# Kernel tuning notes

Hardware: AMD Instinct MI355X
Metric: run time of the kernel (lower is better)

Reference implementation:

```python
import jax, jax.numpy as jnp
import numpy as np

N_NODES = 50000
N_EDGES = 800000
IN_FEATS = 128
OUT_FEATS = 128


def setup_inputs() -> dict:
    key = jax.random.key(0)
    k1, k2, k3, k4 = jax.random.split(key, 4)
    feature = jax.random.normal(k1, (N_NODES, IN_FEATS), dtype=jnp.float32)
    src = jax.random.randint(k2, (N_EDGES,), 0, N_NODES, dtype=jnp.int64)
    dst = jax.random.randint(k3, (N_EDGES,), 0, N_NODES, dtype=jnp.int64)
    # nn.Linear(in_feats, out_feats): W is [out, in], b is [out]
    bound = 1.0 / np.sqrt(IN_FEATS)
    W = jax.random.uniform(k4, (OUT_FEATS, IN_FEATS), minval=-bound, maxval=bound, dtype=jnp.float32)
    b = jnp.zeros((OUT_FEATS,), dtype=jnp.float32)
    return {"feature": feature, "src": src, "dst": dst, "W": W, "b": b}


def reference(feature, src, dst, W, b):
    # DGL update_all(copy_src('h'), sum('m','h')): h'[v] = sum over edges u->v of h[u]
    n_nodes = feature.shape[0]
    msgs = feature[src]  # [E, in_feats] gather
    agg = jax.ops.segment_sum(msgs, dst, num_segments=n_nodes)  # [N, in_feats]
    # linear: agg @ W.T + b
    return jnp.einsum("ni,oi->no", agg, W) + b
```

## Files before the change

kernel.cpp:

```cpp
#include <hip/hip_runtime.h>
#include <hip/hip_bf16.h>

#define N_FEATS 128
#define SCAN_CHUNK 1024

typedef __attribute__((ext_vector_type(8))) short bf16x8;
typedef __attribute__((ext_vector_type(4))) float f32x4;

__device__ __forceinline__ unsigned short f32_to_bf16_rne(float f) {
    unsigned u = __float_as_uint(f);
    u = u + 0x7FFFu + ((u >> 16) & 1u);
    return (unsigned short)(u >> 16);
}

__global__ void gcn_init(const float* __restrict__ W, unsigned short* __restrict__ Wb,
                         int* __restrict__ deg, int n_nodes) {
    int t = blockIdx.x * blockDim.x + threadIdx.x;
    if (t < N_FEATS * N_FEATS / 8) {
        const float4* f4 = reinterpret_cast<const float4*>(W) + (size_t)t * 2;
        float4 x0 = f4[0];
        float4 x1 = f4[1];
        ushort4 o0, o1;
        o0.x = f32_to_bf16_rne(x0.x); o0.y = f32_to_bf16_rne(x0.y);
        o0.z = f32_to_bf16_rne(x0.z); o0.w = f32_to_bf16_rne(x0.w);
        o1.x = f32_to_bf16_rne(x1.x); o1.y = f32_to_bf16_rne(x1.y);
        o1.z = f32_to_bf16_rne(x1.z); o1.w = f32_to_bf16_rne(x1.w);
        reinterpret_cast<ushort4*>(Wb)[(size_t)t * 2 + 0] = o0;
        reinterpret_cast<ushort4*>(Wb)[(size_t)t * 2 + 1] = o1;
    }
    int u = t - N_FEATS * N_FEATS / 8;
    if (u >= 0 && u < n_nodes) deg[u] = 0;
}

__launch_bounds__(256)
__global__ void gcn_transform_mfma(const float* __restrict__ feat,
                                   const unsigned short* __restrict__ Wb,
                                   unsigned short* __restrict__ Y,
                                   int n_nodes) {
    const long long gtid = (long long)blockIdx.x * blockDim.x + threadIdx.x;
    const int wave = (int)(gtid >> 6);
    const int row0 = wave * 16;
    if (row0 >= n_nodes) return;
    const int l = (int)(threadIdx.x & 63);
    const int lr = l & 15;
    const int kb = l >> 4;

    bf16x8 afrag[4] = {};
    if (row0 + lr < n_nodes) {
        const float* aptr = feat + (size_t)(row0 + lr) * N_FEATS + kb * 8;
#pragma unroll
        for (int kk = 0; kk < 4; ++kk) {
            float4 x0 = *reinterpret_cast<const float4*>(aptr + kk * 32);
            float4 x1 = *reinterpret_cast<const float4*>(aptr + kk * 32 + 4);
            bf16x8 af;
            af[0] = (short)f32_to_bf16_rne(x0.x);
            af[1] = (short)f32_to_bf16_rne(x0.y);
            af[2] = (short)f32_to_bf16_rne(x0.z);
            af[3] = (short)f32_to_bf16_rne(x0.w);
            af[4] = (short)f32_to_bf16_rne(x1.x);
            af[5] = (short)f32_to_bf16_rne(x1.y);
            af[6] = (short)f32_to_bf16_rne(x1.z);
            af[7] = (short)f32_to_bf16_rne(x1.w);
            afrag[kk] = af;
        }
    }

    f32x4 acc[8];
#pragma unroll
    for (int nt = 0; nt < 8; ++nt) acc[nt] = (f32x4){0.f, 0.f, 0.f, 0.f};

#pragma unroll
    for (int nt = 0; nt < 8; ++nt) {
        const unsigned short* wp = Wb + (size_t)(nt * 16 + lr) * N_FEATS + kb * 8;
#pragma unroll
        for (int kk = 0; kk < 4; ++kk) {
            bf16x8 bfrag = *reinterpret_cast<const bf16x8*>(wp + kk * 32);
            acc[nt] = __builtin_amdgcn_mfma_f32_16x16x32_bf16(afrag[kk], bfrag, acc[nt], 0, 0, 0);
        }
    }

#pragma unroll
    for (int nt = 0; nt < 8; ++nt) {
        const int col = nt * 16 + lr;
#pragma unroll
        for (int j = 0; j < 4; ++j) {
            const int r = row0 + kb * 4 + j;
            if (r < n_nodes)
                Y[(size_t)r * N_FEATS + col] = f32_to_bf16_rne(acc[nt][j]);
        }
    }
}

__global__ void gcn_hist_pos(const int* __restrict__ src, const int* __restrict__ dst,
                             int* __restrict__ deg, int* __restrict__ pos,
                             int n_edges, int n_nodes) {
    int e = blockIdx.x * blockDim.x + threadIdx.x;
    if (e >= n_edges) return;
    int d = dst[e];
    int s = src[e];
    if ((unsigned)d < (unsigned)n_nodes && (unsigned)s < (unsigned)n_nodes)
        pos[e] = atomicAdd(&deg[d], 1);
}

__launch_bounds__(256)
__global__ void gcn_scan(const int* __restrict__ deg, int* __restrict__ row_start,
                         int n, int nchunks) {
    const int t = threadIdx.x;
    const int b = blockIdx.x;
    const int base = b * SCAN_CHUNK;

    int v = 0;
    for (int j = t; j < base; j += 256) v += deg[j];
    for (int d = 1; d < 64; d <<= 1) v += __shfl_xor(v, d, 64);
    __shared__ int owsum[4];
    __shared__ int s_off;
    if ((t & 63) == 0) owsum[t >> 6] = v;
    __syncthreads();
    if (t == 0) s_off = owsum[0] + owsum[1] + owsum[2] + owsum[3];
    __syncthreads();
    const int chunk_off = s_off;

    const int idx0 = base + t * 4;
    int x[4];
#pragma unroll
    for (int k = 0; k < 4; ++k) {
        int idx = idx0 + k;
        x[k] = (idx < n) ? deg[idx] : 0;
    }
    const int tsum = x[0] + x[1] + x[2] + x[3];

    const int lane = t & 63, w = t >> 6;
    int inc = tsum;
    for (int d = 1; d < 64; d <<= 1) {
        int sv = __shfl_up(inc, d, 64);
        if (lane >= d) inc += sv;
    }
    __shared__ int wsum[4];
    if (lane == 63) wsum[w] = inc;
    __syncthreads();
    int woff = 0;
    for (int i = 0; i < w; ++i) woff += wsum[i];

    int run = chunk_off + woff + inc - tsum;
#pragma unroll
    for (int k = 0; k < 4; ++k) {
        int idx = idx0 + k;
        if (idx < n) row_start[idx] = run;
        run += x[k];
    }

    if (t == 0 && b == nchunks - 1)
        row_start[n] = chunk_off + wsum[0] + wsum[1] + wsum[2] + wsum[3];
}

__global__ void gcn_build_csr_pos(const int* __restrict__ src, const int* __restrict__ dst,
                                  const int* __restrict__ row_start, const int* __restrict__ pos,
                                  int* __restrict__ csr_src, int n_edges, int n_nodes) {
    int e = blockIdx.x * blockDim.x + threadIdx.x;
    if (e >= n_edges) return;
    int d = dst[e];
    int s = src[e];
    if ((unsigned)d >= (unsigned)n_nodes || (unsigned)s >= (unsigned)n_nodes) return;
    csr_src[row_start[d] + pos[e]] = s;
}

#define BACC(acc, v)                                              \
    do {                                                          \
        unsigned uu;                                              \
        uu = (v).x;                                               \
        acc[0] += __uint_as_float(uu << 16);                      \
        acc[1] += __uint_as_float(uu & 0xFFFF0000u);              \
        uu = (v).y;                                               \
        acc[2] += __uint_as_float(uu << 16);                      \
        acc[3] += __uint_as_float(uu & 0xFFFF0000u);              \
        uu = (v).z;                                               \
        acc[4] += __uint_as_float(uu << 16);                      \
        acc[5] += __uint_as_float(uu & 0xFFFF0000u);              \
        uu = (v).w;                                               \
        acc[6] += __uint_as_float(uu << 16);                      \
        acc[7] += __uint_as_float(uu & 0xFFFF0000u);              \
    } while (0)

__launch_bounds__(256)
__global__ void gcn_aggregate_bf16(const uint4* __restrict__ Y,
                                   const int* __restrict__ row_start,
                                   const int* __restrict__ csr_src,
                                   const float* __restrict__ bias,
                                   float* __restrict__ out, int n_nodes) {
    int node = blockIdx.x * 4 + (threadIdx.x >> 6);
    if (node >= n_nodes) return;
    const int l = threadIdx.x & 63;
    const int qw = l >> 4;
    const int ql = l & 15;
    int beg = row_start[node];
    int end = row_start[node + 1];

    float a0[8] = {0,0,0,0,0,0,0,0};
    float a1[8] = {0,0,0,0,0,0,0,0};
    float a2[8] = {0,0,0,0,0,0,0,0};
    float a3[8] = {0,0,0,0,0,0,0,0};

    int i = beg;
    for (; i + 16 <= end; i += 16) {
        int s0 = csr_src[i + qw];
        int s1 = csr_src[i + 4 + qw];
        int s2 = csr_src[i + 8 + qw];
        int s3 = csr_src[i + 12 + qw];
        uint4 v0 = Y[(size_t)s0 * 16 + ql];
        uint4 v1 = Y[(size_t)s1 * 16 + ql];
        uint4 v2 = Y[(size_t)s2 * 16 + ql];
        uint4 v3 = Y[(size_t)s3 * 16 + ql];
        BACC(a0, v0);
        BACC(a1, v1);
        BACC(a2, v2);
        BACC(a3, v3);
    }
    for (; i + 4 <= end; i += 4) {
        int s = csr_src[i + qw];
        uint4 v = Y[(size_t)s * 16 + ql];
        BACC(a0, v);
    }
    int rem = end - i;
    if (qw < rem) {
        int s = csr_src[i + qw];
        uint4 v = Y[(size_t)s * 16 + ql];
        BACC(a0, v);
    }

    float r[8];
#pragma unroll
    for (int k = 0; k < 8; ++k) {
        r[k] = a0[k] + a1[k] + a2[k] + a3[k];
        r[k] += __shfl_xor(r[k], 16, 64);
        r[k] += __shfl_xor(r[k], 32, 64);
    }

    if (qw == 0) {
        const float4 b0 = *reinterpret_cast<const float4*>(bias + ql * 8);
        const float4 b1 = *reinterpret_cast<const float4*>(bias + ql * 8 + 4);
        float4* o4 = reinterpret_cast<float4*>(out + (size_t)node * N_FEATS + ql * 8);
        o4[0] = make_float4(r[0] + b0.x, r[1] + b0.y, r[2] + b0.z, r[3] + b0.w);
        o4[1] = make_float4(r[4] + b1.x, r[5] + b1.y, r[6] + b1.z, r[7] + b1.w);
    }
}

__global__ void gcn_init_c(const float* __restrict__ W, float* __restrict__ Wt) {
    int t = blockIdx.x * blockDim.x + threadIdx.x;
    if (t < N_FEATS * N_FEATS) {
        int o = t >> 7;
        int i = t & 127;
        Wt[i * N_FEATS + o] = W[o * N_FEATS + i];
    }
}

__global__ void gcn_scatter_add(const float* __restrict__ feat,
                                const int* __restrict__ src,
                                const int* __restrict__ dst,
                                float* __restrict__ agg,
                                int n_edges, int n_nodes) {
    long long tid = (long long)blockIdx.x * blockDim.x + threadIdx.x;
    int e = (int)(tid >> 5);
    if (e >= n_edges) return;
    int j = (int)(tid & 31);
    int s = src[e];
    int d = dst[e];
    if ((unsigned)s >= (unsigned)n_nodes || (unsigned)d >= (unsigned)n_nodes) return;
    const float4 v = *reinterpret_cast<const float4*>(feat + (size_t)s * N_FEATS + j * 4);
    float* p = agg + (size_t)d * N_FEATS + j * 4;
    atomicAdd(p + 0, v.x);
    atomicAdd(p + 1, v.y);
    atomicAdd(p + 2, v.z);
    atomicAdd(p + 3, v.w);
}

__launch_bounds__(256)
__global__ void gcn_gemm_inplace(float* __restrict__ out,
                                 const float* __restrict__ Wt,
                                 const float* __restrict__ b,
                                 int n_nodes) {
    __shared__ float a_lds[32 * N_FEATS];

    const int t = threadIdx.x;
    const int node0 = blockIdx.x * 32;
    const int rows = min(32, n_nodes - node0);

    float4* a4 = reinterpret_cast<float4*>(a_lds);
    const float4* out4 = reinterpret_cast<const float4*>(out + (size_t)node0 * N_FEATS);
    const int nflt4 = rows * (N_FEATS / 4);
    for (int idx = t; idx < nflt4; idx += 256) a4[idx] = out4[idx];
    __syncthreads();

    const int oq = t & 31;
    const int ng = t >> 5;

    const float4 bb = reinterpret_cast<const float4*>(b)[oq];
    float4 acc[4];
#pragma unroll
    for (int k = 0; k < 4; ++k) acc[k] = bb;

    const float4* Wt4 = reinterpret_cast<const float4*>(Wt);
#pragma unroll 4
    for (int i = 0; i < N_FEATS; ++i) {
        const float4 w = Wt4[i * 32 + oq];
#pragma unroll
        for (int k = 0; k < 4; ++k) {
            const float a = a_lds[(ng * 4 + k) * N_FEATS + i];
            acc[k].x += a * w.x;
            acc[k].y += a * w.y;
            acc[k].z += a * w.z;
            acc[k].w += a * w.w;
        }
    }

    __syncthreads();

#pragma unroll
    for (int k = 0; k < 4; ++k) {
        const int r = ng * 4 + k;
        if (r < rows) {
            reinterpret_cast<float4*>(out + (size_t)(node0 + r) * N_FEATS)[oq] = acc[k];
        }
    }
}

extern "C" void kernel_launch(void* const* d_in, const int* in_sizes, int n_in,
                              void* d_out, int out_size, void* d_ws, size_t ws_size,
                              hipStream_t stream) {
    const float* feature = (const float*)d_in[0];
    const int*   src     = (const int*)d_in[1];
    const int*   dst     = (const int*)d_in[2];
    const float* W       = (const float*)d_in[3];
    const float* b       = (const float*)d_in[4];
    float* out = (float*)d_out;

    const int n_nodes = in_sizes[0] / N_FEATS;
    const int n_edges = in_sizes[1];
    const int nchunks = (n_nodes + SCAN_CHUNK - 1) / SCAN_CHUNK;

    char* ws = (char*)d_ws;
    size_t off = 0;
    auto take = [&](size_t bytes) -> char* {
        char* p = ws + off;
        off = (off + bytes + 255) & ~(size_t)255;
        return p;
    };
    int* deg       = (int*)take((size_t)n_nodes * sizeof(int));
    int* row_start = (int*)take(((size_t)n_nodes + 1) * sizeof(int));
    int* csr_src   = (int*)take((size_t)n_edges * sizeof(int));
    unsigned short* Yb = (unsigned short*)take((size_t)n_nodes * N_FEATS * sizeof(unsigned short));
    unsigned short* Wb = (unsigned short*)take((size_t)N_FEATS * N_FEATS * sizeof(unsigned short));
    int* pos       = (int*)take((size_t)n_edges * sizeof(int));
    const bool tierA2 = (off <= ws_size);

    if (tierA2) {
        const int init_elems = N_FEATS * N_FEATS / 8 + n_nodes;
        gcn_init<<<(init_elems + 255) / 256, 256, 0, stream>>>(W, Wb, deg, n_nodes);
        const long long nthr = (long long)((n_nodes + 15) / 16) * 64;
        gcn_transform_mfma<<<(int)((nthr + 255) / 256), 256, 0, stream>>>(
            feature, Wb, Yb, n_nodes);
        const int eblocks = (n_edges + 255) / 256;
        gcn_hist_pos<<<eblocks, 256, 0, stream>>>(src, dst, deg, pos, n_edges, n_nodes);
        gcn_scan<<<nchunks, 256, 0, stream>>>(deg, row_start, n_nodes, nchunks);
        gcn_build_csr_pos<<<eblocks, 256, 0, stream>>>(
            src, dst, row_start, pos, csr_src, n_edges, n_nodes);
        gcn_aggregate_bf16<<<(n_nodes + 3) / 4, 256, 0, stream>>>(
            reinterpret_cast<const uint4*>(Yb), row_start, csr_src, b, out, n_nodes);
    } else {
        float* Wt = (float*)d_ws;
        gcn_init_c<<<(N_FEATS * N_FEATS + 255) / 256, 256, 0, stream>>>(W, Wt);
        hipMemsetAsync(d_out, 0, (size_t)n_nodes * N_FEATS * sizeof(float), stream);
        long long total = (long long)n_edges * 32;
        gcn_scatter_add<<<(int)((total + 255) / 256), 256, 0, stream>>>(
            feature, src, dst, out, n_edges, n_nodes);
        gcn_gemm_inplace<<<(n_nodes + 31) / 32, 256, 0, stream>>>(out, Wt, b, n_nodes);
    }
}
```

Baseline: 145.2 us.

## Fuse GCN pipeline into one cooperative persistent kernel with grid syncs

```diff
diff --git a/kernel.cpp b/kernel.cpp
--- a/kernel.cpp
+++ b/kernel.cpp
@@ -1,5 +1,8 @@
 #include <hip/hip_runtime.h>
 #include <hip/hip_bf16.h>
+#include <hip/hip_cooperative_groups.h>
+
+namespace cg = cooperative_groups;
 
 #define N_FEATS 128
 #define SCAN_CHUNK 1024
@@ -13,155 +16,12 @@
     return (unsigned short)(u >> 16);
 }
 
-__global__ void gcn_init(const float* __restrict__ W, unsigned short* __restrict__ Wb,
-                         int* __restrict__ deg, int n_nodes) {
-    int t = blockIdx.x * blockDim.x + threadIdx.x;
-    if (t < N_FEATS * N_FEATS / 8) {
-        const float4* f4 = reinterpret_cast<const float4*>(W) + (size_t)t * 2;
-        float4 x0 = f4[0];
-        float4 x1 = f4[1];
-        ushort4 o0, o1;
-        o0.x = f32_to_bf16_rne(x0.x); o0.y = f32_to_bf16_rne(x0.y);
-        o0.z = f32_to_bf16_rne(x0.z); o0.w = f32_to_bf16_rne(x0.w);
-        o1.x = f32_to_bf16_rne(x1.x); o1.y = f32_to_bf16_rne(x1.y);
-        o1.z = f32_to_bf16_rne(x1.z); o1.w = f32_to_bf16_rne(x1.w);
-        reinterpret_cast<ushort4*>(Wb)[(size_t)t * 2 + 0] = o0;
-        reinterpret_cast<ushort4*>(Wb)[(size_t)t * 2 + 1] = o1;
-    }
-    int u = t - N_FEATS * N_FEATS / 8;
-    if (u >= 0 && u < n_nodes) deg[u] = 0;
-}
-
-__launch_bounds__(256)
-__global__ void gcn_transform_mfma(const float* __restrict__ feat,
-                                   const unsigned short* __restrict__ Wb,
-                                   unsigned short* __restrict__ Y,
-                                   int n_nodes) {
-    const long long gtid = (long long)blockIdx.x * blockDim.x + threadIdx.x;
-    const int wave = (int)(gtid >> 6);
-    const int row0 = wave * 16;
-    if (row0 >= n_nodes) return;
-    const int l = (int)(threadIdx.x & 63);
-    const int lr = l & 15;
-    const int kb = l >> 4;
-
-    bf16x8 afrag[4] = {};
-    if (row0 + lr < n_nodes) {
-        const float* aptr = feat + (size_t)(row0 + lr) * N_FEATS + kb * 8;
-#pragma unroll
-        for (int kk = 0; kk < 4; ++kk) {
-            float4 x0 = *reinterpret_cast<const float4*>(aptr + kk * 32);
-            float4 x1 = *reinterpret_cast<const float4*>(aptr + kk * 32 + 4);
-            bf16x8 af;
-            af[0] = (short)f32_to_bf16_rne(x0.x);
-            af[1] = (short)f32_to_bf16_rne(x0.y);
-            af[2] = (short)f32_to_bf16_rne(x0.z);
-            af[3] = (short)f32_to_bf16_rne(x0.w);
-            af[4] = (short)f32_to_bf16_rne(x1.x);
-            af[5] = (short)f32_to_bf16_rne(x1.y);
-            af[6] = (short)f32_to_bf16_rne(x1.z);
-            af[7] = (short)f32_to_bf16_rne(x1.w);
-            afrag[kk] = af;
-        }
-    }
-
-    f32x4 acc[8];
-#pragma unroll
-    for (int nt = 0; nt < 8; ++nt) acc[nt] = (f32x4){0.f, 0.f, 0.f, 0.f};
-
-#pragma unroll
-    for (int nt = 0; nt < 8; ++nt) {
-        const unsigned short* wp = Wb + (size_t)(nt * 16 + lr) * N_FEATS + kb * 8;
-#pragma unroll
-        for (int kk = 0; kk < 4; ++kk) {
-            bf16x8 bfrag = *reinterpret_cast<const bf16x8*>(wp + kk * 32);
-            acc[nt] = __builtin_amdgcn_mfma_f32_16x16x32_bf16(afrag[kk], bfrag, acc[nt], 0, 0, 0);
-        }
-    }
-
-#pragma unroll
-    for (int nt = 0; nt < 8; ++nt) {
-        const int col = nt * 16 + lr;
-#pragma unroll
-        for (int j = 0; j < 4; ++j) {
-            const int r = row0 + kb * 4 + j;
-            if (r < n_nodes)
-                Y[(size_t)r * N_FEATS + col] = f32_to_bf16_rne(acc[nt][j]);
-        }
-    }
-}
-
-__global__ void gcn_hist_pos(const int* __restrict__ src, const int* __restrict__ dst,
-                             int* __restrict__ deg, int* __restrict__ pos,
-                             int n_edges, int n_nodes) {
-    int e = blockIdx.x * blockDim.x + threadIdx.x;
-    if (e >= n_edges) return;
-    int d = dst[e];
-    int s = src[e];
-    if ((unsigned)d < (unsigned)n_nodes && (unsigned)s < (unsigned)n_nodes)
-        pos[e] = atomicAdd(&deg[d], 1);
-}
-
-__launch_bounds__(256)
-__global__ void gcn_scan(const int* __restrict__ deg, int* __restrict__ row_start,
-                         int n, int nchunks) {
-    const int t = threadIdx.x;
-    const int b = blockIdx.x;
-    const int base = b * SCAN_CHUNK;
-
-    int v = 0;
-    for (int j = t; j < base; j += 256) v += deg[j];
-    for (int d = 1; d < 64; d <<= 1) v += __shfl_xor(v, d, 64);
-    __shared__ int owsum[4];
-    __shared__ int s_off;
-    if ((t & 63) == 0) owsum[t >> 6] = v;
-    __syncthreads();
-    if (t == 0) s_off = owsum[0] + owsum[1] + owsum[2] + owsum[3];
-    __syncthreads();
-    const int chunk_off = s_off;
-
-    const int idx0 = base + t * 4;
-    int x[4];
-#pragma unroll
-    for (int k = 0; k < 4; ++k) {
-        int idx = idx0 + k;
-        x[k] = (idx < n) ? deg[idx] : 0;
-    }
-    const int tsum = x[0] + x[1] + x[2] + x[3];
-
-    const int lane = t & 63, w = t >> 6;
-    int inc = tsum;
-    for (int d = 1; d < 64; d <<= 1) {
-        int sv = __shfl_up(inc, d, 64);
-        if (lane >= d) inc += sv;
-    }
-    __shared__ int wsum[4];
-    if (lane == 63) wsum[w] = inc;
-    __syncthreads();
-    int woff = 0;
-    for (int i = 0; i < w; ++i) woff += wsum[i];
-
-    int run = chunk_off + woff + inc - tsum;
-#pragma unroll
-    for (int k = 0; k < 4; ++k) {
-        int idx = idx0 + k;
-        if (idx < n) row_start[idx] = run;
-        run += x[k];
-    }
-
-    if (t == 0 && b == nchunks - 1)
-        row_start[n] = chunk_off + wsum[0] + wsum[1] + wsum[2] + wsum[3];
-}
-
-__global__ void gcn_build_csr_pos(const int* __restrict__ src, const int* __restrict__ dst,
-                                  const int* __restrict__ row_start, const int* __restrict__ pos,
-                                  int* __restrict__ csr_src, int n_edges, int n_nodes) {
-    int e = blockIdx.x * blockDim.x + threadIdx.x;
-    if (e >= n_edges) return;
-    int d = dst[e];
-    int s = src[e];
-    if ((unsigned)d >= (unsigned)n_nodes || (unsigned)s >= (unsigned)n_nodes) return;
-    csr_src[row_start[d] + pos[e]] = s;
+__device__ __forceinline__ void cast8(const float4& x0, const float4& x1,
+                                      ushort4& o0, ushort4& o1) {
+    o0.x = f32_to_bf16_rne(x0.x); o0.y = f32_to_bf16_rne(x0.y);
+    o0.z = f32_to_bf16_rne(x0.z); o0.w = f32_to_bf16_rne(x0.w);
+    o1.x = f32_to_bf16_rne(x1.x); o1.y = f32_to_bf16_rne(x1.y);
+    o1.z = f32_to_bf16_rne(x1.z); o1.w = f32_to_bf16_rne(x1.w);
 }
 
 #define BACC(acc, v)                                              \
@@ -181,6 +41,341 @@
         acc[7] += __uint_as_float(uu & 0xFFFF0000u);              \
     } while (0)
 
+__launch_bounds__(256, 4)
+__global__ void gcn_mega(const float* __restrict__ feat, const float* __restrict__ W,
+                         const int* __restrict__ src, const int* __restrict__ dst,
+                         const float* __restrict__ bias, float* __restrict__ out,
+                         int* __restrict__ deg, int* __restrict__ row_start,
+                         int* __restrict__ pos, int* __restrict__ csr_src,
+                         unsigned short* __restrict__ Wb, unsigned short* __restrict__ Y,
+                         int n_nodes, int n_edges, int nchunks) {
+    cg::grid_group grid = cg::this_grid();
+    const int t = threadIdx.x;
+    const int gsize = gridDim.x * 256;
+    const int gtid = blockIdx.x * 256 + t;
+
+    for (int i = gtid; i < N_FEATS * N_FEATS / 8; i += gsize) {
+        const float4* f4 = reinterpret_cast<const float4*>(W) + (size_t)i * 2;
+        float4 x0 = f4[0], x1 = f4[1];
+        ushort4 o0, o1;
+        cast8(x0, x1, o0, o1);
+        reinterpret_cast<ushort4*>(Wb)[(size_t)i * 2 + 0] = o0;
+        reinterpret_cast<ushort4*>(Wb)[(size_t)i * 2 + 1] = o1;
+    }
+    for (int i = gtid; i < n_nodes; i += gsize) deg[i] = 0;
+    grid.sync();
+
+    {
+        const int wid = gtid >> 6;
+        const int nwv = gsize >> 6;
+        const int lw = t & 63;
+        const int lr = lw & 15;
+        const int kb = lw >> 4;
+        const int ntile = (n_nodes + 15) >> 4;
+        for (int tl = wid; tl < ntile; tl += nwv) {
+            const int row0 = tl << 4;
+            bf16x8 afrag[4] = {};
+            if (row0 + lr < n_nodes) {
+                const float* aptr = feat + (size_t)(row0 + lr) * N_FEATS + kb * 8;
+#pragma unroll
+                for (int kk = 0; kk < 4; ++kk) {
+                    float4 x0 = *reinterpret_cast<const float4*>(aptr + kk * 32);
+                    float4 x1 = *reinterpret_cast<const float4*>(aptr + kk * 32 + 4);
+                    ushort4 o0, o1;
+                    cast8(x0, x1, o0, o1);
+                    bf16x8 af;
+                    af[0] = (short)o0.x; af[1] = (short)o0.y;
+                    af[2] = (short)o0.z; af[3] = (short)o0.w;
+                    af[4] = (short)o1.x; af[5] = (short)o1.y;
+                    af[6] = (short)o1.z; af[7] = (short)o1.w;
+                    afrag[kk] = af;
+                }
+            }
+            f32x4 acc[8];
+#pragma unroll
+            for (int nt = 0; nt < 8; ++nt) acc[nt] = (f32x4){0.f, 0.f, 0.f, 0.f};
+#pragma unroll
+            for (int nt = 0; nt < 8; ++nt) {
+                const unsigned short* wp = Wb + (size_t)(nt * 16 + lr) * N_FEATS + kb * 8;
+#pragma unroll
+                for (int kk = 0; kk < 4; ++kk) {
+                    bf16x8 bfrag = *reinterpret_cast<const bf16x8*>(wp + kk * 32);
+                    acc[nt] = __builtin_amdgcn_mfma_f32_16x16x32_bf16(afrag[kk], bfrag,
+                                                                      acc[nt], 0, 0, 0);
+                }
+            }
+#pragma unroll
+            for (int nt = 0; nt < 8; ++nt) {
+                const int col = nt * 16 + lr;
+#pragma unroll
+                for (int j = 0; j < 4; ++j) {
+                    const int r = row0 + kb * 4 + j;
+                    if (r < n_nodes)
+                        Y[(size_t)r * N_FEATS + col] = f32_to_bf16_rne(acc[nt][j]);
+                }
+            }
+        }
+    }
+    for (int e = gtid; e < n_edges; e += gsize) {
+        int d = dst[e];
+        int s = src[e];
+        if ((unsigned)d < (unsigned)n_nodes && (unsigned)s < (unsigned)n_nodes)
+            pos[e] = atomicAdd(&deg[d], 1);
+    }
+    grid.sync();
+
+    if ((int)blockIdx.x < nchunks) {
+        const int b = blockIdx.x;
+        const int base = b * SCAN_CHUNK;
+        int v = 0;
+        for (int j = t; j < base; j += 256) v += deg[j];
+        for (int d = 1; d < 64; d <<= 1) v += __shfl_xor(v, d, 64);
+        __shared__ int owsum[4];
+        __shared__ int s_off;
+        if ((t & 63) == 0) owsum[t >> 6] = v;
+        __syncthreads();
+        if (t == 0) s_off = owsum[0] + owsum[1] + owsum[2] + owsum[3];
+        __syncthreads();
+        const int chunk_off = s_off;
+
+        const int idx0 = base + t * 4;
+        int x[4];
+#pragma unroll
+        for (int k = 0; k < 4; ++k) {
+            int idx = idx0 + k;
+            x[k] = (idx < n_nodes) ? deg[idx] : 0;
+        }
+        const int tsum = x[0] + x[1] + x[2] + x[3];
+        const int lane = t & 63, w = t >> 6;
+        int inc = tsum;
+        for (int d = 1; d < 64; d <<= 1) {
+            int sv = __shfl_up(inc, d, 64);
+            if (lane >= d) inc += sv;
+        }
+        __shared__ int wsum[4];
+        if (lane == 63) wsum[w] = inc;
+        __syncthreads();
+        int woff = 0;
+        for (int i = 0; i < w; ++i) woff += wsum[i];
+
+        int run = chunk_off + woff + inc - tsum;
+#pragma unroll
+        for (int k = 0; k < 4; ++k) {
+            int idx = idx0 + k;
+            if (idx < n_nodes) row_start[idx] = run;
+            run += x[k];
+        }
+        if (t == 0 && b == nchunks - 1)
+            row_start[n_nodes] = chunk_off + wsum[0] + wsum[1] + wsum[2] + wsum[3];
+    }
+    grid.sync();
+
+    for (int e = gtid; e < n_edges; e += gsize) {
+        int d = dst[e];
+        int s = src[e];
+        if ((unsigned)d < (unsigned)n_nodes && (unsigned)s < (unsigned)n_nodes)
+            csr_src[row_start[d] + pos[e]] = s;
+    }
+    grid.sync();
+
+    {
+        const int wid = gtid >> 6;
+        const int nwv = gsize >> 6;
+        const int lw = t & 63;
+        const int qw = lw >> 4;
+        const int ql = lw & 15;
+        const uint4* Y4 = reinterpret_cast<const uint4*>(Y);
+        for (int node = wid; node < n_nodes; node += nwv) {
+            const int beg = row_start[node];
+            const int end = row_start[node + 1];
+            float a0[8] = {0,0,0,0,0,0,0,0};
+            float a1[8] = {0,0,0,0,0,0,0,0};
+            float a2[8] = {0,0,0,0,0,0,0,0};
+            float a3[8] = {0,0,0,0,0,0,0,0};
+            int i = beg;
+            for (; i + 16 <= end; i += 16) {
+                int s0 = csr_src[i + qw];
+                int s1 = csr_src[i + 4 + qw];
+                int s2 = csr_src[i + 8 + qw];
+                int s3 = csr_src[i + 12 + qw];
+                uint4 v0 = Y4[(size_t)s0 * 16 + ql];
+                uint4 v1 = Y4[(size_t)s1 * 16 + ql];
+                uint4 v2 = Y4[(size_t)s2 * 16 + ql];
+                uint4 v3 = Y4[(size_t)s3 * 16 + ql];
+                BACC(a0, v0);
+                BACC(a1, v1);
+                BACC(a2, v2);
+                BACC(a3, v3);
+            }
+            for (; i + 4 <= end; i += 4) {
+                int s = csr_src[i + qw];
+                uint4 v = Y4[(size_t)s * 16 + ql];
+                BACC(a0, v);
+            }
+            int rem = end - i;
+            if (qw < rem) {
+                int s = csr_src[i + qw];
+                uint4 v = Y4[(size_t)s * 16 + ql];
+                BACC(a0, v);
+            }
+            float r[8];
+#pragma unroll
+            for (int k = 0; k < 8; ++k) {
+                r[k] = a0[k] + a1[k] + a2[k] + a3[k];
+                r[k] += __shfl_xor(r[k], 16, 64);
+                r[k] += __shfl_xor(r[k], 32, 64);
+            }
+            if (qw == 0) {
+                const float4 b0 = *reinterpret_cast<const float4*>(bias + ql * 8);
+                const float4 b1 = *reinterpret_cast<const float4*>(bias + ql * 8 + 4);
+                float4* o4 = reinterpret_cast<float4*>(out + (size_t)node * N_FEATS + ql * 8);
+                o4[0] = make_float4(r[0] + b0.x, r[1] + b0.y, r[2] + b0.z, r[3] + b0.w);
+                o4[1] = make_float4(r[4] + b1.x, r[5] + b1.y, r[6] + b1.z, r[7] + b1.w);
+            }
+        }
+    }
+}
+
+__global__ void gcn_init(const float* __restrict__ W, unsigned short* __restrict__ Wb,
+                         int* __restrict__ deg, int n_nodes) {
+    int t = blockIdx.x * blockDim.x + threadIdx.x;
+    if (t < N_FEATS * N_FEATS / 8) {
+        const float4* f4 = reinterpret_cast<const float4*>(W) + (size_t)t * 2;
+        float4 x0 = f4[0], x1 = f4[1];
+        ushort4 o0, o1;
+        cast8(x0, x1, o0, o1);
+        reinterpret_cast<ushort4*>(Wb)[(size_t)t * 2 + 0] = o0;
+        reinterpret_cast<ushort4*>(Wb)[(size_t)t * 2 + 1] = o1;
+    }
+    int u = t - N_FEATS * N_FEATS / 8;
+    if (u >= 0 && u < n_nodes) deg[u] = 0;
+}
+
+__launch_bounds__(256)
+__global__ void gcn_transform_mfma(const float* __restrict__ feat,
+                                   const unsigned short* __restrict__ Wb,
+                                   unsigned short* __restrict__ Y,
+                                   int n_nodes) {
+    const long long gtid = (long long)blockIdx.x * blockDim.x + threadIdx.x;
+    const int wave = (int)(gtid >> 6);
+    const int row0 = wave * 16;
+    if (row0 >= n_nodes) return;
+    const int l = (int)(threadIdx.x & 63);
+    const int lr = l & 15;
+    const int kb = l >> 4;
+
+    bf16x8 afrag[4] = {};
+    if (row0 + lr < n_nodes) {
+        const float* aptr = feat + (size_t)(row0 + lr) * N_FEATS + kb * 8;
+#pragma unroll
+        for (int kk = 0; kk < 4; ++kk) {
+            float4 x0 = *reinterpret_cast<const float4*>(aptr + kk * 32);
+            float4 x1 = *reinterpret_cast<const float4*>(aptr + kk * 32 + 4);
+            ushort4 o0, o1;
+            cast8(x0, x1, o0, o1);
+            bf16x8 af;
+            af[0] = (short)o0.x; af[1] = (short)o0.y;
+            af[2] = (short)o0.z; af[3] = (short)o0.w;
+            af[4] = (short)o1.x; af[5] = (short)o1.y;
+            af[6] = (short)o1.z; af[7] = (short)o1.w;
+            afrag[kk] = af;
+        }
+    }
+    f32x4 acc[8];
+#pragma unroll
+    for (int nt = 0; nt < 8; ++nt) acc[nt] = (f32x4){0.f, 0.f, 0.f, 0.f};
+#pragma unroll
+    for (int nt = 0; nt < 8; ++nt) {
+        const unsigned short* wp = Wb + (size_t)(nt * 16 + lr) * N_FEATS + kb * 8;
+#pragma unroll
+        for (int kk = 0; kk < 4; ++kk) {
+            bf16x8 bfrag = *reinterpret_cast<const bf16x8*>(wp + kk * 32);
+            acc[nt] = __builtin_amdgcn_mfma_f32_16x16x32_bf16(afrag[kk], bfrag, acc[nt], 0, 0, 0);
+        }
+    }
+#pragma unroll
+    for (int nt = 0; nt < 8; ++nt) {
+        const int col = nt * 16 + lr;
+#pragma unroll
+        for (int j = 0; j < 4; ++j) {
+            const int r = row0 + kb * 4 + j;
+            if (r < n_nodes)
+                Y[(size_t)r * N_FEATS + col] = f32_to_bf16_rne(acc[nt][j]);
+        }
+    }
+}
+
+__global__ void gcn_hist_pos(const int* __restrict__ src, const int* __restrict__ dst,
+                             int* __restrict__ deg, int* __restrict__ pos,
+                             int n_edges, int n_nodes) {
+    int e = blockIdx.x * blockDim.x + threadIdx.x;
+    if (e >= n_edges) return;
+    int d = dst[e];
+    int s = src[e];
+    if ((unsigned)d < (unsigned)n_nodes && (unsigned)s < (unsigned)n_nodes)
+        pos[e] = atomicAdd(&deg[d], 1);
+}
+
+__launch_bounds__(256)
+__global__ void gcn_scan(const int* __restrict__ deg, int* __restrict__ row_start,
+                         int n, int nchunks) {
+    const int t = threadIdx.x;
+    const int b = blockIdx.x;
+    const int base = b * SCAN_CHUNK;
+
+    int v = 0;
+    for (int j = t; j < base; j += 256) v += deg[j];
+    for (int d = 1; d < 64; d <<= 1) v += __shfl_xor(v, d, 64);
+    __shared__ int owsum[4];
+    __shared__ int s_off;
+    if ((t & 63) == 0) owsum[t >> 6] = v;
+    __syncthreads();
+    if (t == 0) s_off = owsum[0] + owsum[1] + owsum[2] + owsum[3];
+    __syncthreads();
+    const int chunk_off = s_off;
+
+    const int idx0 = base + t * 4;
+    int x[4];
+#pragma unroll
+    for (int k = 0; k < 4; ++k) {
+        int idx = idx0 + k;
+        x[k] = (idx < n) ? deg[idx] : 0;
+    }
+    const int tsum = x[0] + x[1] + x[2] + x[3];
+    const int lane = t & 63, w = t >> 6;
+    int inc = tsum;
+    for (int d = 1; d < 64; d <<= 1) {
+        int sv = __shfl_up(inc, d, 64);
+        if (lane >= d) inc += sv;
+    }
+    __shared__ int wsum[4];
+    if (lane == 63) wsum[w] = inc;
+    __syncthreads();
+    int woff = 0;
+    for (int i = 0; i < w; ++i) woff += wsum[i];
+
+    int run = chunk_off + woff + inc - tsum;
+#pragma unroll
+    for (int k = 0; k < 4; ++k) {
+        int idx = idx0 + k;
+        if (idx < n) row_start[idx] = run;
+        run += x[k];
+    }
+    if (t == 0 && b == nchunks - 1)
+        row_start[n] = chunk_off + wsum[0] + wsum[1] + wsum[2] + wsum[3];
+}
+
+__global__ void gcn_build_csr_pos(const int* __restrict__ src, const int* __restrict__ dst,
+                                  const int* __restrict__ row_start, const int* __restrict__ pos,
+                                  int* __restrict__ csr_src, int n_edges, int n_nodes) {
+    int e = blockIdx.x * blockDim.x + threadIdx.x;
+    if (e >= n_edges) return;
+    int d = dst[e];
+    int s = src[e];
+    if ((unsigned)d >= (unsigned)n_nodes || (unsigned)s >= (unsigned)n_nodes) return;
+    csr_src[row_start[d] + pos[e]] = s;
+}
+
 __launch_bounds__(256)
 __global__ void gcn_aggregate_bf16(const uint4* __restrict__ Y,
                                    const int* __restrict__ row_start,
@@ -234,7 +429,6 @@
         r[k] += __shfl_xor(r[k], 16, 64);
         r[k] += __shfl_xor(r[k], 32, 64);
     }
-
     if (qw == 0) {
         const float4 b0 = *reinterpret_cast<const float4*>(bias + ql * 8);
         const float4 b1 = *reinterpret_cast<const float4*>(bias + ql * 8 + 4);
@@ -279,7 +473,6 @@
                                  const float* __restrict__ b,
                                  int n_nodes) {
     __shared__ float a_lds[32 * N_FEATS];
-
     const int t = threadIdx.x;
     const int node0 = blockIdx.x * 32;
     const int rows = min(32, n_nodes - node0);
@@ -292,7 +485,6 @@
 
     const int oq = t & 31;
     const int ng = t >> 5;
-
     const float4 bb = reinterpret_cast<const float4*>(b)[oq];
     float4 acc[4];
 #pragma unroll
@@ -311,15 +503,12 @@
             acc[k].w += a * w.w;
         }
     }
-
     __syncthreads();
-
 #pragma unroll
     for (int k = 0; k < 4; ++k) {
         const int r = ng * 4 + k;
-        if (r < rows) {
+        if (r < rows)
             reinterpret_cast<float4*>(out + (size_t)(node0 + r) * N_FEATS)[oq] = acc[k];
-        }
     }
 }
 
@@ -333,9 +522,9 @@
     const float* b       = (const float*)d_in[4];
     float* out = (float*)d_out;
 
-    const int n_nodes = in_sizes[0] / N_FEATS;
-    const int n_edges = in_sizes[1];
-    const int nchunks = (n_nodes + SCAN_CHUNK - 1) / SCAN_CHUNK;
+    int n_nodes = in_sizes[0] / N_FEATS;
+    int n_edges = in_sizes[1];
+    int nchunks = (n_nodes + SCAN_CHUNK - 1) / SCAN_CHUNK;
 
     char* ws = (char*)d_ws;
     size_t off = 0;
@@ -353,18 +542,26 @@
     const bool tierA2 = (off <= ws_size);
 
     if (tierA2) {
-        const int init_elems = N_FEATS * N_FEATS / 8 + n_nodes;
-        gcn_init<<<(init_elems + 255) / 256, 256, 0, stream>>>(W, Wb, deg, n_nodes);
-        const long long nthr = (long long)((n_nodes + 15) / 16) * 64;
-        gcn_transform_mfma<<<(int)((nthr + 255) / 256), 256, 0, stream>>>(
-            feature, Wb, Yb, n_nodes);
-        const int eblocks = (n_edges + 255) / 256;
-        gcn_hist_pos<<<eblocks, 256, 0, stream>>>(src, dst, deg, pos, n_edges, n_nodes);
-        gcn_scan<<<nchunks, 256, 0, stream>>>(deg, row_start, n_nodes, nchunks);
-        gcn_build_csr_pos<<<eblocks, 256, 0, stream>>>(
-            src, dst, row_start, pos, csr_src, n_edges, n_nodes);
-        gcn_aggregate_bf16<<<(n_nodes + 3) / 4, 256, 0, stream>>>(
-            reinterpret_cast<const uint4*>(Yb), row_start, csr_src, b, out, n_nodes);
+        void* args[] = {(void*)&feature, (void*)&W, (void*)&src, (void*)&dst,
+                        (void*)&b, (void*)&out, (void*)&deg, (void*)&row_start,
+                        (void*)&pos, (void*)&csr_src, (void*)&Wb, (void*)&Yb,
+                        (void*)&n_nodes, (void*)&n_edges, (void*)&nchunks};
+        hipError_t err = hipLaunchCooperativeKernel((void*)gcn_mega, dim3(1024),
+                                                    dim3(256), args, 0, stream);
+        if (err != hipSuccess) {
+            const int init_elems = N_FEATS * N_FEATS / 8 + n_nodes;
+            gcn_init<<<(init_elems + 255) / 256, 256, 0, stream>>>(W, Wb, deg, n_nodes);
+            const long long nthr = (long long)((n_nodes + 15) / 16) * 64;
+            gcn_transform_mfma<<<(int)((nthr + 255) / 256), 256, 0, stream>>>(
+                feature, Wb, Yb, n_nodes);
+            const int eblocks = (n_edges + 255) / 256;
+            gcn_hist_pos<<<eblocks, 256, 0, stream>>>(src, dst, deg, pos, n_edges, n_nodes);
+            gcn_scan<<<nchunks, 256, 0, stream>>>(deg, row_start, n_nodes, nchunks);
+            gcn_build_csr_pos<<<eblocks, 256, 0, stream>>>(
+                src, dst, row_start, pos, csr_src, n_edges, n_nodes);
+            gcn_aggregate_bf16<<<(n_nodes + 3) / 4, 256, 0, stream>>>(
+                reinterpret_cast<const uint4*>(Yb), row_start, csr_src, b, out, n_nodes);
+        }
     } else {
         float* Wt = (float*)d_ws;
         gcn_init_c<<<(N_FEATS * N_FEATS + 255) / 256, 256, 0, stream>>>(W, Wt);
```

After: 544.4 us. +274.9%, slower.
